# Kernel optimization log

Hardware: AMD Instinct MI355X
Metric: run time of the kernel (lower is better)

Reference implementation:

```python
import jax, jax.numpy as jnp
import numpy as np

BOS = 1          # BOS_TOK_IDX
PAD = 0          # PAD_TOK_IDX (embedding padding row zeroed)
NL = 2           # n_layers (both decoder and encoder)
H_DEC = 1024     # decoder hidden = enc.emb_size
H_ENC = 512      # encoder hidden per direction (out_size = 1024)


def lstm_cell(x, h, c, Wih, Whh, bih, bhh):
    # PyTorch gate order: i, f, g, o
    gates = x @ Wih.T + h @ Whh.T + bih + bhh
    i, f, g, o = jnp.split(gates, 4, axis=-1)
    c = jax.nn.sigmoid(f) * c + jax.nn.sigmoid(i) * jnp.tanh(g)
    h = jax.nn.sigmoid(o) * jnp.tanh(c)
    return h, c


def setup_inputs() -> dict:
    key = jax.random.key(0)
    ks = jax.random.split(key, 20)
    B, T_ENC, V, E = 32, 128, 32000, 512
    sd = 1.0 / np.sqrt(H_DEC)
    se = 1.0 / np.sqrt(H_ENC)
    u = lambda k, shape, s: jax.random.uniform(k, shape, jnp.float32, -s, s)
    emb_W = jax.random.normal(ks[0], (V, E), jnp.float32)
    emb_W = emb_W.at[PAD].set(0.0)  # padding_idx
    return {
        "enc_outs": jax.random.normal(ks[1], (B, T_ENC, 2 * H_ENC), jnp.float32),
        "enc_h": 0.1 * jax.random.normal(ks[2], (NL, B, H_DEC), jnp.float32),
        "enc_c": 0.1 * jax.random.normal(ks[3], (NL, B, H_DEC), jnp.float32),
        "max_len": 256,
        "emb_W": emb_W,
        # decoder LSTM (unidirectional, 2 layers; layer0 in=E, layer1 in=H_DEC)
        "dec_Wih0": u(ks[4], (4 * H_DEC, E), sd),
        "dec_Whh0": u(ks[5], (4 * H_DEC, H_DEC), sd),
        "dec_bih0": u(ks[6], (4 * H_DEC,), sd),
        "dec_bhh0": u(ks[7], (4 * H_DEC,), sd),
        "dec_Wih1": u(ks[8], (4 * H_DEC, H_DEC), sd),
        "dec_Whh1": u(ks[9], (4 * H_DEC, H_DEC), sd),
        "dec_bih1": u(ks[10], (4 * H_DEC,), sd),
        "dec_bhh1": u(ks[11], (4 * H_DEC,), sd),
        # encoder biLSTM, stacked [layer, dir]; input dim 1024 for both layers
        "enc_Wih": u(ks[12], (NL, 2, 4 * H_ENC, 2 * H_ENC), se),
        "enc_Whh": u(ks[13], (NL, 2, 4 * H_ENC, H_ENC), se),
        "enc_bih": u(ks[14], (NL, 2, 4 * H_ENC), se),
        "enc_bhh": u(ks[15], (NL, 2, 4 * H_ENC), se),
    }


def _run_dir(x, Wih, Whh, bih, bhh, reverse):
    # x: [B, T, D] -> ys: [B, T, H], final (h, c)
    B = x.shape[0]
    H = Whh.shape[-1]
    z = jnp.zeros((B, H), dtype=x.dtype)

    def step(carry, xt):
        h, c = lstm_cell(xt, carry[0], carry[1], Wih, Whh, bih, bhh)
        return (h, c), h

    (hT, cT), ys = jax.lax.scan(step, (z, z), jnp.swapaxes(x, 0, 1), reverse=reverse)
    return jnp.swapaxes(ys, 0, 1), hT, cT


def reference(enc_outs, enc_h, enc_c, max_len, emb_W,
              dec_Wih0, dec_Whh0, dec_bih0, dec_bhh0,
              dec_Wih1, dec_Whh1, dec_bih1, dec_bhh1,
              enc_Wih, enc_Whh, enc_bih, enc_bhh):
    B = enc_outs.shape[0]
    # dec_inps is never updated in the loop: always the BOS embedding (eval dropout = id)
    x0 = jnp.broadcast_to(emb_W[BOS], (B, emb_W.shape[1]))

    def dec_step(carry, _):
        h0, c0, h1, c1 = carry
        h0, c0 = lstm_cell(x0, h0, c0, dec_Wih0, dec_Whh0, dec_bih0, dec_bhh0)
        h1, c1 = lstm_cell(h0, h1, c1, dec_Wih1, dec_Whh1, dec_bih1, dec_bhh1)
        return (h0, c0, h1, c1), h1

    init = (enc_h[0], enc_c[0], enc_h[1], enc_c[1])
    _, result = jax.lax.scan(dec_step, init, None, length=max_len)  # [T, B, H_DEC]
    out = jnp.swapaxes(result, 0, 1)  # [B, T, H_DEC]

    # bidirectional encoder over the decoded sequence (pre_embedded, full lengths)
    for l in range(NL):
        yf, hf, cf = _run_dir(out, enc_Wih[l, 0], enc_Whh[l, 0], enc_bih[l, 0], enc_bhh[l, 0], False)
        yb, hb, cb = _run_dir(out, enc_Wih[l, 1], enc_Whh[l, 1], enc_bih[l, 1], enc_bhh[l, 1], True)
        out = jnp.concatenate([yf, yb], axis=-1)

    # to_dec_state: concat last-layer fwd/bwd states, expand over n_layers
    lnhn = jnp.concatenate([hf, hb], axis=1)  # [B, out_size]
    lncn = jnp.concatenate([cf, cb], axis=1)
    dec_h = jnp.broadcast_to(lnhn, (NL,) + lnhn.shape)
    dec_c = jnp.broadcast_to(lncn, (NL,) + lncn.shape)
    return out, dec_h, dec_c
```

## Files before the change

### kernel.cpp

```cpp
#include <hip/hip_runtime.h>


typedef _Float16 f16;
typedef _Float16 hvec8 __attribute__((ext_vector_type(8)));
typedef float fvec4 __attribute__((ext_vector_type(4)));

#define WS_H1   135168
#define WS_HE   266240
#define WS_DEC  397312
#define WS_Y0   17174528

__device__ __forceinline__ fvec4 mf(hvec8 a, hvec8 b, fvec4 c) {
    return __builtin_amdgcn_mfma_f32_16x16x32_f16(a, b, c, 0, 0, 0);
}

__device__ __forceinline__ hvec8 ldb8(const float* p) {
    hvec8 h;
#pragma unroll
    for (int j = 0; j < 8; ++j) h[j] = (f16)p[j];
    return h;
}

__device__ __forceinline__ hvec8 lda8(const f16* p) {
    hvec8 v;
    asm volatile("global_load_dwordx4 %0, %1, off sc1" : "=v"(v) : "v"(p));
    return v;
}
__device__ __forceinline__ void vm_wait() {
    asm volatile("s_waitcnt vmcnt(0)" ::: "memory");
    __builtin_amdgcn_sched_barrier(0);
}

__device__ __forceinline__ void st2(f16* p, float a, float b) {
    union { f16 h[2]; unsigned u; } x;
    x.h[0] = (f16)a; x.h[1] = (f16)b;
    __hip_atomic_store((unsigned*)p, x.u, __ATOMIC_RELAXED, __HIP_MEMORY_SCOPE_AGENT);
}

__device__ __forceinline__ float sigf(float x) { return 1.f / (1.f + __expf(-x)); }
__device__ __forceinline__ float thf(float x) {
    x = fminf(15.f, fmaxf(-15.f, x));
    float e = __expf(2.f * x);
    return (e - 1.f) / (e + 1.f);
}

#define RED(t, m, w, n)  red[(((t)*16 + (m))*132) + ((w)*16) + (n)]

__device__ __forceinline__ float sum8(const float* p) {
    return ((p[0] + p[16]) + (p[32] + p[48])) + ((p[64] + p[80]) + (p[96] + p[112]));
}

__global__ void __launch_bounds__(512, 1)
seq2seq_kernel(const float* __restrict__ enc_h, const float* __restrict__ enc_c,
               const float* __restrict__ emb_W,
               const float* __restrict__ dWih0, const float* __restrict__ dWhh0,
               const float* __restrict__ dbih0, const float* __restrict__ dbhh0,
               const float* __restrict__ dWih1, const float* __restrict__ dWhh1,
               const float* __restrict__ dbih1, const float* __restrict__ dbhh1,
               const float* __restrict__ eWih, const float* __restrict__ eWhh,
               const float* __restrict__ ebih, const float* __restrict__ ebhh,
               float* __restrict__ out, char* __restrict__ ws)
{
    const int tid  = threadIdx.x;
    const int wave = tid >> 6, lane = tid & 63;
    const int wg   = blockIdx.x;
    const int bg   = wg >> 7;
    const int layer= (wg >> 6) & 1;
    const int g2   = wg & 63;
    const int n16  = lane & 15;
    const int kq   = (lane >> 4) * 8;
    const int m    = n16;

    unsigned* flags  = (unsigned*)(out + 8388608);
    unsigned* myflag = flags + (size_t)wg * 64;

    f16* H1  = (f16*)(ws + WS_H1);
    f16* HE  = (f16*)(ws + WS_HE);
    f16* DEC = (f16*)(ws + WS_DEC);
    f16* Y0  = (f16*)(ws + WS_Y0);
    f16* H0R = Y0;

    __shared__ float red[64 * 132];
    __shared__ float cst[16][16];
    __shared__ float bias_l[64];

    unsigned cnt = 0;
    auto barpollW = [&](int base, int width, unsigned tgt) {
        if (lane == 0)
            __hip_atomic_store(myflag, tgt, __ATOMIC_RELAXED, __HIP_MEMORY_SCOPE_AGENT);
        const unsigned* p0 = flags + (size_t)(base + (lane & (width - 1))) * 64;
        for (;;) {
            unsigned a = __hip_atomic_load(p0, __ATOMIC_RELAXED, __HIP_MEMORY_SCOPE_AGENT);
            if (width > 64) {
                unsigned b = __hip_atomic_load(p0 + 64 * 64, __ATOMIC_RELAXED, __HIP_MEMORY_SCOPE_AGENT);
                a = a < b ? a : b;
                if (width > 128) {
                    unsigned c2 = __hip_atomic_load(p0 + 128 * 64, __ATOMIC_RELAXED, __HIP_MEMORY_SCOPE_AGENT);
                    unsigned d2 = __hip_atomic_load(p0 + 192 * 64, __ATOMIC_RELAXED, __HIP_MEMORY_SCOPE_AGENT);
                    a = a < c2 ? a : c2;
                    a = a < d2 ? a : d2;
                }
            }
            if (__all((int)(a >= tgt))) break;
            __builtin_amdgcn_s_sleep(1);
        }
    };
    auto barpoll2 = [&](int ownbase, int othbase, unsigned tgt, unsigned otgt) {
        if (lane == 0)
            __hip_atomic_store(myflag, tgt, __ATOMIC_RELAXED, __HIP_MEMORY_SCOPE_AGENT);
        const unsigned* p0 = flags + (size_t)(ownbase + lane) * 64;
        const unsigned* q0 = flags + (size_t)(othbase + lane) * 64;
        for (;;) {
            unsigned a = __hip_atomic_load(p0, __ATOMIC_RELAXED, __HIP_MEMORY_SCOPE_AGENT);
            unsigned b = __hip_atomic_load(q0, __ATOMIC_RELAXED, __HIP_MEMORY_SCOPE_AGENT);
            if (__all((int)((a >= tgt) && (b >= otgt)))) break;
            __builtin_amdgcn_s_sleep(1);
        }
    };

    const int u0 = g2 * 16;
    hvec8 bW[4][8];
    {
        const int gate = n16 >> 2, uu = n16 & 3;
        if (layer == 0) {
#pragma unroll
            for (int t = 0; t < 4; ++t) {
                const int r = gate * 1024 + u0 + t * 4 + uu;
#pragma unroll
                for (int s = 0; s < 4; ++s)
                    bW[t][s] = ldb8(dWhh0 + (size_t)r * 1024 + wave * 128 + s * 32 + kq);
            }
        } else {
#pragma unroll
            for (int t = 0; t < 4; ++t) {
                const int r = gate * 1024 + u0 + t * 4 + uu;
#pragma unroll
                for (int s = 0; s < 8; ++s) {
                    const int k1 = wave * 256 + s * 32;
                    bW[t][s] = (k1 < 1024)
                        ? ldb8(dWih1 + (size_t)r * 1024 + k1 + kq)
                        : ldb8(dWhh1 + (size_t)r * 1024 + (k1 - 1024) + kq);
                }
            }
        }
    }
    if (tid < 128) {
        const int j = tid >> 4, mm = tid & 15;
        const int b = bg * 16 + mm, u = u0 + 2 * j;
        const float* sc = enc_c + (size_t)(layer * 32 + b) * 1024 + u;
        const float* sh = enc_h + (size_t)(layer * 32 + b) * 1024 + u;
        cst[2 * j][mm]     = sc[0];
        cst[2 * j + 1][mm] = sc[1];
        if (layer == 0) st2(H0R + (size_t)(3 * 32 + b) * 1024 + u, sh[0], sh[1]);
        else            st2(H1  + (size_t)(32 + b) * 1024 + u, sh[0], sh[1]);
    }
    if (tid < 64) {
        const int t = tid >> 4, nn = tid & 15;
        const int r = (nn >> 2) * 1024 + u0 + t * 4 + (nn & 3);
        if (layer == 0) {
            const float* x0 = emb_W + 512;
            float s = dbih0[r] + dbhh0[r];
            const float* wr = dWih0 + (size_t)r * 512;
            for (int k = 0; k < 512; ++k) s += wr[k] * x0[k];
            bias_l[tid] = s;
        } else {
            bias_l[tid] = dbih1[r] + dbhh1[r];
        }
    }
    const int L0base = bg * 128, L1base = bg * 128 + 64;
    const int ownbase = layer ? L1base : L0base;
    const int othbase = layer ? L0base : L1base;
    __syncthreads();
    ++cnt;
    if (wave == 0) barpoll2(ownbase, othbase, cnt, cnt);
    __syncthreads();

    for (int n = 0; n <= 256; ++n) {
        const int prd = (n + 1) & 1;
        const int pwr = n & 1;
        const bool act = layer ? (n >= 1) : (n < 256);
        fvec4 acc[4];
#pragma unroll
        for (int i = 0; i < 4; ++i) acc[i] = 0;
        if (act) {
            hvec8 af[8];
            if (layer == 0) {
                const f16* a0 = H0R + (size_t)((((n - 1) & 3)) * 32 + bg * 16 + m) * 1024
                              + wave * 128 + kq;
#pragma unroll
                for (int s = 0; s < 4; ++s) af[s] = lda8(a0 + s * 32);
                vm_wait();
#pragma unroll
                for (int s = 0; s < 4; ++s)
#pragma unroll
                    for (int t = 0; t < 4; ++t) acc[t] = mf(af[s], bW[t][s], acc[t]);
            } else {
                const f16* b0 = H0R + (size_t)((((n - 1) & 3)) * 32 + bg * 16 + m) * 1024;
                const f16* b1 = H1 + (size_t)(pwr * 32 + bg * 16 + m) * 1024;
#pragma unroll
                for (int s = 0; s < 8; ++s) {
                    const int k1 = wave * 256 + s * 32;
                    af[s] = lda8(k1 < 1024 ? b0 + k1 + kq : b1 + (k1 - 1024) + kq);
                }
                vm_wait();
#pragma unroll
                for (int s = 0; s < 8; ++s)
#pragma unroll
                    for (int t = 0; t < 4; ++t) acc[t] = mf(af[s], bW[t][s], acc[t]);
            }
        }
        {
            const int mg = lane >> 4;
#pragma unroll
            for (int t = 0; t < 4; ++t)
#pragma unroll
                for (int r2 = 0; r2 < 4; ++r2)
                    RED(t, mg * 4 + r2, wave, n16) = acc[t][r2];
        }
        __syncthreads();
        float s0 = 0.f, s1 = 0.f;
        int   sm2 = 0, sj = 0;
        if (tid >= 64 && tid < 192 && act) {
            const int q = tid - 64;
            const int j = q >> 4, m2 = q & 15;
            float hh[2];
#pragma unroll
            for (int e = 0; e < 2; ++e) {
                const int uu = 2 * j + e, tt = uu >> 2, ul = uu & 3;
                const float* p = &RED(tt, m2, 0, ul);
                const float gi = sum8(p)      + bias_l[tt * 16 + ul];
                const float gf = sum8(p + 4)  + bias_l[tt * 16 + 4 + ul];
                const float gg = sum8(p + 8)  + bias_l[tt * 16 + 8 + ul];
                const float go = sum8(p + 12) + bias_l[tt * 16 + 12 + ul];
                float c = cst[uu][m2];
                c = sigf(gf) * c + sigf(gi) * thf(gg);
                hh[e] = sigf(go) * thf(c);
                cst[uu][m2] = c;
            }
            const int b = bg * 16 + m2, u = u0 + 2 * j;
            if (layer == 0) {
                st2(H0R + (size_t)((n & 3) * 32 + b) * 1024 + u, hh[0], hh[1]);
            } else {
                st2(H1 + (size_t)(prd * 32 + b) * 1024 + u, hh[0], hh[1]);
                s0 = hh[0]; s1 = hh[1]; sm2 = m2; sj = j;
            }
        }
        __syncthreads();
        ++cnt;
        if (wave == 0) {
            if (layer == 0) barpoll2(L0base, L1base, cnt, cnt < 2 ? 0u : cnt - 2);
            else            barpoll2(L1base, L0base, cnt, cnt);
        } else if (layer == 1 && tid >= 64 && tid < 192 && n >= 1) {
            st2(DEC + ((size_t)(n - 1) * 32 + bg * 16 + sm2) * 1024 + u0 + 2 * sj, s0, s1);
        }
        __syncthreads();
    }

    ++cnt;
    if (wave == 0) barpollW(0, 256, cnt);
    __syncthreads();
    if (wg >= 128) return;

    const int bg2 = wg >> 6;
    const int dir = (wg >> 5) & 1;
    const int ge  = wg & 31;
    const int ue0 = ge * 16;
    const int dbase = bg2 * 64 + dir * 32;
    float fdh0 = 0.f, fdh1 = 0.f, fdc0 = 0.f, fdc1 = 0.f;
    int   fdm2 = 0, fdj = 0;
    for (int l = 0; l < 2; ++l) {
        hvec8 bE[4][6];
        {
            const int gate = n16 >> 2, uu = n16 & 3;
            const float* Wih = eWih + (size_t)(l * 2 + dir) * 2048 * 1024;
            const float* Whh = eWhh + (size_t)(l * 2 + dir) * 2048 * 512;
#pragma unroll
            for (int t = 0; t < 4; ++t) {
                const int r = gate * 512 + ue0 + t * 4 + uu;
#pragma unroll
                for (int s = 0; s < 6; ++s) {
                    const int kb = wave * 192 + s * 32;
                    bE[t][s] = (kb < 1024)
                        ? ldb8(Wih + (size_t)r * 1024 + kb + kq)
                        : ldb8(Whh + (size_t)r * 512 + (kb - 1024) + kq);
                }
            }
        }
        if (tid < 64) {
            const int t = tid >> 4, nn = tid & 15;
            const int r = (nn >> 2) * 512 + ue0 + t * 4 + (nn & 3);
            bias_l[tid] = ebih[(size_t)(l * 2 + dir) * 2048 + r]
                        + ebhh[(size_t)(l * 2 + dir) * 2048 + r];
        }
        if (tid < 128) {
            const int j = tid >> 4, mm = tid & 15;
            cst[2 * j][mm] = 0.f;
            cst[2 * j + 1][mm] = 0.f;
            st2(HE + (size_t)((dir * 2 + 1) * 32 + bg2 * 16 + mm) * 512 + ue0 + 2 * j, 0.f, 0.f);
        }
        __syncthreads();
        ++cnt;
        if (wave == 0) barpollW(dbase, 32, cnt);
        __syncthreads();
        const f16* yprev = (l == 0) ? DEC : Y0;
        hvec8 ypf[6];
        {
            const int t0 = dir ? 255 : 0;
            const int b = bg2 * 16 + n16;
#pragma unroll
            for (int s = 0; s < 6; ++s) {
                const int kb = wave * 192 + s * 32;
                if (kb < 1024)
                    ypf[s] = lda8(yprev + ((size_t)t0 * 32 + b) * 1024 + kb + kq);
            }
        }
        for (int tau = 0; tau < 256; ++tau) {
            const int t = dir ? (255 - tau) : tau;
            const int prd = (tau + 1) & 1, pwr = tau & 1;
            const int b = bg2 * 16 + n16;
            hvec8 hef[6];
#pragma unroll
            for (int s = 0; s < 6; ++s) {
                const int kb = wave * 192 + s * 32;
                if (kb >= 1024)
                    hef[s] = lda8(HE + (size_t)((dir * 2 + prd) * 32 + b) * 512 + (kb - 1024) + kq);
            }
            vm_wait();
            fvec4 acc2[4];
#pragma unroll
            for (int i = 0; i < 4; ++i) acc2[i] = 0;
#pragma unroll
            for (int s = 0; s < 6; ++s) {
                const int kb = wave * 192 + s * 32;
                const hvec8 a = (kb < 1024) ? ypf[s] : hef[s];
                acc2[0] = mf(a, bE[0][s], acc2[0]);
                acc2[1] = mf(a, bE[1][s], acc2[1]);
                acc2[2] = mf(a, bE[2][s], acc2[2]);
                acc2[3] = mf(a, bE[3][s], acc2[3]);
            }
            if (tau < 255) {
                const int tn = dir ? (t - 1) : (t + 1);
#pragma unroll
                for (int s = 0; s < 6; ++s) {
                    const int kb = wave * 192 + s * 32;
                    if (kb < 1024)
                        ypf[s] = lda8(yprev + ((size_t)tn * 32 + b) * 1024 + kb + kq);
                }
            }
            const int mg = lane >> 4;
#pragma unroll
            for (int tt = 0; tt < 4; ++tt)
#pragma unroll
                for (int r2 = 0; r2 < 4; ++r2)
                    RED(tt, mg * 4 + r2, wave, n16) = acc2[tt][r2];
            __syncthreads();
            float dh0 = 0.f, dh1 = 0.f, dc0 = 0.f, dc1 = 0.f;
            int   dm2 = 0, dj = 0;
            if (tid >= 64 && tid < 192) {
                const int q = tid - 64;
                const int j = q >> 4, m2 = q & 15;
                float hh[2], cc[2];
#pragma unroll
                for (int e = 0; e < 2; ++e) {
                    const int uu = 2 * j + e, tt = uu >> 2, ul = uu & 3;
                    const float* p = &RED(tt, m2, 0, ul);
                    const float gi = sum8(p)      + bias_l[tt * 16 + ul];
                    const float gf = sum8(p + 4)  + bias_l[tt * 16 + 4 + ul];
                    const float gg = sum8(p + 8)  + bias_l[tt * 16 + 8 + ul];
                    const float go = sum8(p + 12) + bias_l[tt * 16 + 12 + ul];
                    float c = cst[uu][m2];
                    c = sigf(gf) * c + sigf(gi) * thf(gg);
                    hh[e] = sigf(go) * thf(c);
                    cc[e] = c;
                    cst[uu][m2] = c;
                }
                st2(HE + (size_t)((dir * 2 + pwr) * 32 + bg2 * 16 + m2) * 512 + ue0 + 2 * j,
                    hh[0], hh[1]);
                dh0 = hh[0]; dh1 = hh[1]; dc0 = cc[0]; dc1 = cc[1];
                dm2 = m2; dj = j;
            }
            __syncthreads();
            ++cnt;
            if (wave == 0) {
                if (!(l == 1 && tau == 255)) barpollW(dbase, 32, cnt);
            } else if (tid >= 64 && tid < 192) {
                const int b2 = bg2 * 16 + dm2, u = ue0 + 2 * dj;
                if (l == 0) {
                    st2(Y0 + ((size_t)t * 32 + b2) * 1024 + dir * 512 + u, dh0, dh1);
                } else {
                    float* o = out + ((size_t)b2 * 256 + t) * 1024 + dir * 512 + u;
                    o[0] = dh0; o[1] = dh1;
                    if (tau == 255) {
                        fdh0 = dh0; fdh1 = dh1;
                        fdc0 = dc0; fdc1 = dc1;
                        fdm2 = dm2; fdj = dj;
                    }
                }
            }
            __syncthreads();
        }
        if (l == 0) {
            __syncthreads();
            ++cnt;
            if (wave == 0) barpollW(bg2 * 64, 64, cnt);
            __syncthreads();
        }
    }
    __syncthreads();
    ++cnt;
    if (wave == 0) barpollW(0, 128, cnt);
    __syncthreads();
    if (tid >= 64 && tid < 192) {
        const int b2 = bg2 * 16 + fdm2;
        const int col = dir * 512 + ue0 + 2 * fdj;
        float* oh = out + 8388608 + (size_t)b2 * 1024 + col;
        float* oc = out + 8454144 + (size_t)b2 * 1024 + col;
        oh[0] = fdh0; oh[1] = fdh1;
        oh[32768] = fdh0; oh[32769] = fdh1;
        oc[0] = fdc0; oc[1] = fdc1;
        oc[32768] = fdc0; oc[32769] = fdc1;
    }
}

extern "C" void kernel_launch(void* const* d_in, const int* in_sizes, int n_in,
                              void* d_out, int out_size, void* d_ws, size_t ws_size,
                              hipStream_t stream) {
    (void)in_sizes; (void)n_in; (void)out_size; (void)ws_size;
    const float* enc_h = (const float*)d_in[1];
    const float* enc_c = (const float*)d_in[2];
    const float* emb_W = (const float*)d_in[4];
    const float* dWih0 = (const float*)d_in[5];
    const float* dWhh0 = (const float*)d_in[6];
    const float* dbih0 = (const float*)d_in[7];
    const float* dbhh0 = (const float*)d_in[8];
    const float* dWih1 = (const float*)d_in[9];
    const float* dWhh1 = (const float*)d_in[10];
    const float* dbih1 = (const float*)d_in[11];
    const float* dbhh1 = (const float*)d_in[12];
    const float* eWih  = (const float*)d_in[13];
    const float* eWhh  = (const float*)d_in[14];
    const float* ebih  = (const float*)d_in[15];
    const float* ebhh  = (const float*)d_in[16];
    float* outp = (float*)d_out;
    char* ws = (char*)d_ws;

    hipMemsetAsync((char*)d_out + 33554432, 0, 65536, stream);

    void* args[] = {&enc_h, &enc_c, &emb_W, &dWih0, &dWhh0, &dbih0, &dbhh0,
                    &dWih1, &dWhh1, &dbih1, &dbhh1, &eWih, &eWhh, &ebih, &ebhh,
                    &outp, &ws};
    hipLaunchCooperativeKernel((const void*)seq2seq_kernel, dim3(256), dim3(512),
                               args, 0, stream);
}
```

Before: 3.146 ms.

## Halve grid and interleave two batch halves with per-half flag barriers

Instead of assigning each 16-row batch group to separate workgroups (256 WGs), each of 128 WGs now processes both batch halves alternately, keeping two cell-state sets and two flag words per WG. Barriers become per-half point-to-point flags, so one half's compute can overlap another half's cross-WG synchronisation latency, and the DEC store moves into the compute path. This trades parallelism (half the CUs) for hiding barrier latency, and the encoder drops its Y prefetch in favour of loading the input each step.

```diff
diff --git a/kernel.cpp b/kernel.cpp
--- a/kernel.cpp
+++ b/kernel.cpp
@@ -64,8 +64,7 @@
     const int tid  = threadIdx.x;
     const int wave = tid >> 6, lane = tid & 63;
     const int wg   = blockIdx.x;
-    const int bg   = wg >> 7;
-    const int layer= (wg >> 6) & 1;
+    const int layer= wg >> 6;
     const int g2   = wg & 63;
     const int n16  = lane & 15;
     const int kq   = (lane >> 4) * 8;
@@ -81,41 +80,14 @@
     f16* H0R = Y0;
 
     __shared__ float red[64 * 132];
-    __shared__ float cst[16][16];
+    __shared__ float cst[2][16][16];
     __shared__ float bias_l[64];
 
-    unsigned cnt = 0;
-    auto barpollW = [&](int base, int width, unsigned tgt) {
-        if (lane == 0)
-            __hip_atomic_store(myflag, tgt, __ATOMIC_RELAXED, __HIP_MEMORY_SCOPE_AGENT);
-        const unsigned* p0 = flags + (size_t)(base + (lane & (width - 1))) * 64;
-        for (;;) {
-            unsigned a = __hip_atomic_load(p0, __ATOMIC_RELAXED, __HIP_MEMORY_SCOPE_AGENT);
-            if (width > 64) {
-                unsigned b = __hip_atomic_load(p0 + 64 * 64, __ATOMIC_RELAXED, __HIP_MEMORY_SCOPE_AGENT);
-                a = a < b ? a : b;
-                if (width > 128) {
-                    unsigned c2 = __hip_atomic_load(p0 + 128 * 64, __ATOMIC_RELAXED, __HIP_MEMORY_SCOPE_AGENT);
-                    unsigned d2 = __hip_atomic_load(p0 + 192 * 64, __ATOMIC_RELAXED, __HIP_MEMORY_SCOPE_AGENT);
-                    a = a < c2 ? a : c2;
-                    a = a < d2 ? a : d2;
-                }
-            }
-            if (__all((int)(a >= tgt))) break;
-            __builtin_amdgcn_s_sleep(1);
-        }
+    auto stflag = [&](int word, unsigned v) {
+        __hip_atomic_store(myflag + word * 16, v, __ATOMIC_RELAXED, __HIP_MEMORY_SCOPE_AGENT);
     };
-    auto barpoll2 = [&](int ownbase, int othbase, unsigned tgt, unsigned otgt) {
-        if (lane == 0)
-            __hip_atomic_store(myflag, tgt, __ATOMIC_RELAXED, __HIP_MEMORY_SCOPE_AGENT);
-        const unsigned* p0 = flags + (size_t)(ownbase + lane) * 64;
-        const unsigned* q0 = flags + (size_t)(othbase + lane) * 64;
-        for (;;) {
-            unsigned a = __hip_atomic_load(p0, __ATOMIC_RELAXED, __HIP_MEMORY_SCOPE_AGENT);
-            unsigned b = __hip_atomic_load(q0, __ATOMIC_RELAXED, __HIP_MEMORY_SCOPE_AGENT);
-            if (__all((int)((a >= tgt) && (b >= otgt)))) break;
-            __builtin_amdgcn_s_sleep(1);
-        }
+    auto ldflag = [&](const unsigned* p) {
+        return __hip_atomic_load(p, __ATOMIC_RELAXED, __HIP_MEMORY_SCOPE_AGENT);
     };
 
     const int u0 = g2 * 16;
@@ -146,13 +118,16 @@
     }
     if (tid < 128) {
         const int j = tid >> 4, mm = tid & 15;
-        const int b = bg * 16 + mm, u = u0 + 2 * j;
-        const float* sc = enc_c + (size_t)(layer * 32 + b) * 1024 + u;
-        const float* sh = enc_h + (size_t)(layer * 32 + b) * 1024 + u;
-        cst[2 * j][mm]     = sc[0];
-        cst[2 * j + 1][mm] = sc[1];
-        if (layer == 0) st2(H0R + (size_t)(3 * 32 + b) * 1024 + u, sh[0], sh[1]);
-        else            st2(H1  + (size_t)(32 + b) * 1024 + u, sh[0], sh[1]);
+#pragma unroll
+        for (int s = 0; s < 2; ++s) {
+            const int b = s * 16 + mm, u = u0 + 2 * j;
+            const float* sc = enc_c + (size_t)(layer * 32 + b) * 1024 + u;
+            const float* sh = enc_h + (size_t)(layer * 32 + b) * 1024 + u;
+            cst[s][2 * j][mm]     = sc[0];
+            cst[s][2 * j + 1][mm] = sc[1];
+            if (layer == 0) st2(H0R + (size_t)(3 * 32 + b) * 1024 + u, sh[0], sh[1]);
+            else            st2(H1  + (size_t)(32 + b) * 1024 + u, sh[0], sh[1]);
+        }
     }
     if (tid < 64) {
         const int t = tid >> 4, nn = tid & 15;
@@ -167,46 +142,52 @@
             bias_l[tid] = dbih1[r] + dbhh1[r];
         }
     }
-    const int L0base = bg * 128, L1base = bg * 128 + 64;
-    const int ownbase = layer ? L1base : L0base;
-    const int othbase = layer ? L0base : L1base;
+    const int ownbase = layer * 64, othbase = (layer ^ 1) * 64;
     __syncthreads();
-    ++cnt;
-    if (wave == 0) barpoll2(ownbase, othbase, cnt, cnt);
-    __syncthreads();
-
-    for (int n = 0; n <= 256; ++n) {
-        const int prd = (n + 1) & 1;
-        const int pwr = n & 1;
+    if (wave == 0) {
+        if (lane == 0) { stflag(0, 1u); stflag(1, 1u); }
+        const unsigned* p0 = flags + (size_t)(ownbase + lane) * 64;
+        for (;;) {
+            unsigned a = ldflag(p0), b = ldflag(p0 + 16);
+            if (__all((int)(a >= 1u && b >= 1u))) break;
+            __builtin_amdgcn_s_sleep(1);
+        }
+    }
+
+    for (int i = 0; i < 514; ++i) {
+        const int s = i & 1, n = i >> 1;
         const bool act = layer ? (n >= 1) : (n < 256);
+        __syncthreads();
+        if (wave == 0 && lane == 0 && i > 0)
+            stflag(s ^ 1, (unsigned)(((i - 1) >> 1) + 2));
         fvec4 acc[4];
 #pragma unroll
-        for (int i = 0; i < 4; ++i) acc[i] = 0;
+        for (int t = 0; t < 4; ++t) acc[t] = 0;
         if (act) {
             hvec8 af[8];
             if (layer == 0) {
-                const f16* a0 = H0R + (size_t)((((n - 1) & 3)) * 32 + bg * 16 + m) * 1024
+                const f16* a0 = H0R + (size_t)(((n - 1) & 3) * 32 + s * 16 + m) * 1024
                               + wave * 128 + kq;
 #pragma unroll
-                for (int s = 0; s < 4; ++s) af[s] = lda8(a0 + s * 32);
+                for (int sN = 0; sN < 4; ++sN) af[sN] = lda8(a0 + sN * 32);
                 vm_wait();
 #pragma unroll
-                for (int s = 0; s < 4; ++s)
-#pragma unroll
-                    for (int t = 0; t < 4; ++t) acc[t] = mf(af[s], bW[t][s], acc[t]);
+                for (int sN = 0; sN < 4; ++sN)
+#pragma unroll
+                    for (int t = 0; t < 4; ++t) acc[t] = mf(af[sN], bW[t][sN], acc[t]);
             } else {
-                const f16* b0 = H0R + (size_t)((((n - 1) & 3)) * 32 + bg * 16 + m) * 1024;
-                const f16* b1 = H1 + (size_t)(pwr * 32 + bg * 16 + m) * 1024;
-#pragma unroll
-                for (int s = 0; s < 8; ++s) {
-                    const int k1 = wave * 256 + s * 32;
-                    af[s] = lda8(k1 < 1024 ? b0 + k1 + kq : b1 + (k1 - 1024) + kq);
+                const f16* b0 = H0R + (size_t)(((n - 1) & 3) * 32 + s * 16 + m) * 1024;
+                const f16* b1 = H1 + (size_t)((n & 1) * 32 + s * 16 + m) * 1024;
+#pragma unroll
+                for (int sN = 0; sN < 8; ++sN) {
+                    const int k1 = wave * 256 + sN * 32;
+                    af[sN] = lda8(k1 < 1024 ? b0 + k1 + kq : b1 + (k1 - 1024) + kq);
                 }
                 vm_wait();
 #pragma unroll
-                for (int s = 0; s < 8; ++s)
-#pragma unroll
-                    for (int t = 0; t < 4; ++t) acc[t] = mf(af[s], bW[t][s], acc[t]);
+                for (int sN = 0; sN < 8; ++sN)
+#pragma unroll
+                    for (int t = 0; t < 4; ++t) acc[t] = mf(af[sN], bW[t][sN], acc[t]);
             }
         }
         {
@@ -218,9 +199,7 @@
                     RED(t, mg * 4 + r2, wave, n16) = acc[t][r2];
         }
         __syncthreads();
-        float s0 = 0.f, s1 = 0.f;
-        int   sm2 = 0, sj = 0;
-        if (tid >= 64 && tid < 192 && act) {
+        if (act && tid >= 64 && tid < 192) {
             const int q = tid - 64;
             const int j = q >> 4, m2 = q & 15;
             float hh[2];
@@ -232,42 +211,53 @@
                 const float gf = sum8(p + 4)  + bias_l[tt * 16 + 4 + ul];
                 const float gg = sum8(p + 8)  + bias_l[tt * 16 + 8 + ul];
                 const float go = sum8(p + 12) + bias_l[tt * 16 + 12 + ul];
-                float c = cst[uu][m2];
+                float c = cst[s][uu][m2];
                 c = sigf(gf) * c + sigf(gi) * thf(gg);
                 hh[e] = sigf(go) * thf(c);
-                cst[uu][m2] = c;
-            }
-            const int b = bg * 16 + m2, u = u0 + 2 * j;
+                cst[s][uu][m2] = c;
+            }
+            const int b = s * 16 + m2, u = u0 + 2 * j;
             if (layer == 0) {
                 st2(H0R + (size_t)((n & 3) * 32 + b) * 1024 + u, hh[0], hh[1]);
             } else {
-                st2(H1 + (size_t)(prd * 32 + b) * 1024 + u, hh[0], hh[1]);
-                s0 = hh[0]; s1 = hh[1]; sm2 = m2; sj = j;
-            }
-        }
-        __syncthreads();
-        ++cnt;
-        if (wave == 0) {
-            if (layer == 0) barpoll2(L0base, L1base, cnt, cnt < 2 ? 0u : cnt - 2);
-            else            barpoll2(L1base, L0base, cnt, cnt);
-        } else if (layer == 1 && tid >= 64 && tid < 192 && n >= 1) {
-            st2(DEC + ((size_t)(n - 1) * 32 + bg * 16 + sm2) * 1024 + u0 + 2 * sj, s0, s1);
-        }
-        __syncthreads();
-    }
-
-    ++cnt;
-    if (wave == 0) barpollW(0, 256, cnt);
+                st2(H1 + (size_t)(((n + 1) & 1) * 32 + b) * 1024 + u, hh[0], hh[1]);
+                st2(DEC + ((size_t)(n - 1) * 32 + b) * 1024 + u, hh[0], hh[1]);
+            }
+        }
+        if (wave == 0 && i + 1 < 514) {
+            const int s2 = (i + 1) & 1, n2 = (i + 1) >> 1;
+            const unsigned town = (unsigned)(n2 + 1);
+            const unsigned toth = layer ? (unsigned)(n2 + 1) : (unsigned)n2;
+            const unsigned* p0 = flags + (size_t)(ownbase + lane) * 64 + s2 * 16;
+            const unsigned* q0 = flags + (size_t)(othbase + lane) * 64 + s2 * 16;
+            for (;;) {
+                unsigned a = ldflag(p0), b = ldflag(q0);
+                if (__all((int)(a >= town && b >= toth))) break;
+                __builtin_amdgcn_s_sleep(1);
+            }
+        }
+    }
+
     __syncthreads();
-    if (wg >= 128) return;
-
-    const int bg2 = wg >> 6;
-    const int dir = (wg >> 5) & 1;
-    const int ge  = wg & 31;
+    if (wave == 0) {
+        if (lane == 0) { stflag(0, 259u); stflag(1, 259u); }
+        const unsigned* p0 = flags + (size_t)lane * 64;
+        const unsigned* p1 = p0 + (size_t)64 * 64;
+        for (;;) {
+            unsigned a = ldflag(p0), b = ldflag(p1);
+            if (__all((int)(a >= 259u && b >= 259u))) break;
+            __builtin_amdgcn_s_sleep(1);
+        }
+    }
+    __syncthreads();
+    if (wg >= 64) return;
+
+    const int dir = wg >> 5, ge = wg & 31;
     const int ue0 = ge * 16;
-    const int dbase = bg2 * 64 + dir * 32;
-    float fdh0 = 0.f, fdh1 = 0.f, fdc0 = 0.f, fdc1 = 0.f;
-    int   fdm2 = 0, fdj = 0;
+    const int dbase = dir * 32;
+    float f0h0 = 0.f, f0h1 = 0.f, f0c0 = 0.f, f0c1 = 0.f;
+    float f1h0 = 0.f, f1h1 = 0.f, f1c0 = 0.f, f1c1 = 0.f;
+    unsigned EB = 260;
     for (int l = 0; l < 2; ++l) {
         hvec8 bE[4][6];
         {
@@ -278,9 +268,9 @@
             for (int t = 0; t < 4; ++t) {
                 const int r = gate * 512 + ue0 + t * 4 + uu;
 #pragma unroll
-                for (int s = 0; s < 6; ++s) {
-                    const int kb = wave * 192 + s * 32;
-                    bE[t][s] = (kb < 1024)
+                for (int sN = 0; sN < 6; ++sN) {
+                    const int kb = wave * 192 + sN * 32;
+                    bE[t][sN] = (kb < 1024)
                         ? ldb8(Wih + (size_t)r * 1024 + kb + kq)
                         : ldb8(Whh + (size_t)r * 512 + (kb - 1024) + kq);
                 }
@@ -294,68 +284,60 @@
         }
         if (tid < 128) {
             const int j = tid >> 4, mm = tid & 15;
-            cst[2 * j][mm] = 0.f;
-            cst[2 * j + 1][mm] = 0.f;
-            st2(HE + (size_t)((dir * 2 + 1) * 32 + bg2 * 16 + mm) * 512 + ue0 + 2 * j, 0.f, 0.f);
+#pragma unroll
+            for (int s = 0; s < 2; ++s) {
+                cst[s][2 * j][mm] = 0.f;
+                cst[s][2 * j + 1][mm] = 0.f;
+                st2(HE + (size_t)((dir * 2 + 1) * 32 + s * 16 + mm) * 512 + ue0 + 2 * j,
+                    0.f, 0.f);
+            }
         }
         __syncthreads();
-        ++cnt;
-        if (wave == 0) barpollW(dbase, 32, cnt);
-        __syncthreads();
-        const f16* yprev = (l == 0) ? DEC : Y0;
-        hvec8 ypf[6];
-        {
-            const int t0 = dir ? 255 : 0;
-            const int b = bg2 * 16 + n16;
-#pragma unroll
-            for (int s = 0; s < 6; ++s) {
-                const int kb = wave * 192 + s * 32;
-                if (kb < 1024)
-                    ypf[s] = lda8(yprev + ((size_t)t0 * 32 + b) * 1024 + kb + kq);
-            }
-        }
-        for (int tau = 0; tau < 256; ++tau) {
+        if (wave == 0) {
+            if (lane == 0) { stflag(0, EB); stflag(1, EB); }
+            const unsigned* p0 = flags + (size_t)(dbase + (lane & 31)) * 64;
+            for (;;) {
+                unsigned a = ldflag(p0);
+                if (__all((int)(a >= EB))) break;
+                __builtin_amdgcn_s_sleep(1);
+            }
+        }
+        const f16* yprev = l ? Y0 : DEC;
+        for (int j2 = 0; j2 < 512; ++j2) {
+            const int s = j2 & 1, tau = j2 >> 1;
             const int t = dir ? (255 - tau) : tau;
             const int prd = (tau + 1) & 1, pwr = tau & 1;
-            const int b = bg2 * 16 + n16;
-            hvec8 hef[6];
-#pragma unroll
-            for (int s = 0; s < 6; ++s) {
-                const int kb = wave * 192 + s * 32;
-                if (kb >= 1024)
-                    hef[s] = lda8(HE + (size_t)((dir * 2 + prd) * 32 + b) * 512 + (kb - 1024) + kq);
+            __syncthreads();
+            if (wave == 0 && lane == 0 && j2 > 0)
+                stflag(s ^ 1, EB + (unsigned)(((j2 - 1) >> 1) + 1));
+            const int b = s * 16 + n16;
+            hvec8 af[6];
+#pragma unroll
+            for (int sN = 0; sN < 6; ++sN) {
+                const int kb = wave * 192 + sN * 32;
+                const f16* p = (kb < 1024)
+                    ? yprev + ((size_t)t * 32 + b) * 1024 + kb + kq
+                    : HE + (size_t)((dir * 2 + prd) * 32 + b) * 512 + (kb - 1024) + kq;
+                af[sN] = lda8(p);
             }
             vm_wait();
             fvec4 acc2[4];
 #pragma unroll
-            for (int i = 0; i < 4; ++i) acc2[i] = 0;
-#pragma unroll
-            for (int s = 0; s < 6; ++s) {
-                const int kb = wave * 192 + s * 32;
-                const hvec8 a = (kb < 1024) ? ypf[s] : hef[s];
-                acc2[0] = mf(a, bE[0][s], acc2[0]);
-                acc2[1] = mf(a, bE[1][s], acc2[1]);
-                acc2[2] = mf(a, bE[2][s], acc2[2]);
-                acc2[3] = mf(a, bE[3][s], acc2[3]);
-            }
-            if (tau < 255) {
-                const int tn = dir ? (t - 1) : (t + 1);
-#pragma unroll
-                for (int s = 0; s < 6; ++s) {
-                    const int kb = wave * 192 + s * 32;
-                    if (kb < 1024)
-                        ypf[s] = lda8(yprev + ((size_t)tn * 32 + b) * 1024 + kb + kq);
-                }
-            }
-            const int mg = lane >> 4;
-#pragma unroll
-            for (int tt = 0; tt < 4; ++tt)
-#pragma unroll
-                for (int r2 = 0; r2 < 4; ++r2)
-                    RED(tt, mg * 4 + r2, wave, n16) = acc2[tt][r2];
+            for (int t2 = 0; t2 < 4; ++t2) acc2[t2] = 0;
+#pragma unroll
+            for (int sN = 0; sN < 6; ++sN)
+#pragma unroll
+                for (int t2 = 0; t2 < 4; ++t2)
+                    acc2[t2] = mf(af[sN], bE[t2][sN], acc2[t2]);
+            {
+                const int mg = lane >> 4;
+#pragma unroll
+                for (int t2 = 0; t2 < 4; ++t2)
+#pragma unroll
+                    for (int r2 = 0; r2 < 4; ++r2)
+                        RED(t2, mg * 4 + r2, wave, n16) = acc2[t2][r2];
+            }
             __syncthreads();
-            float dh0 = 0.f, dh1 = 0.f, dc0 = 0.f, dc1 = 0.f;
-            int   dm2 = 0, dj = 0;
             if (tid >= 64 && tid < 192) {
                 const int q = tid - 64;
                 const int j = q >> 4, m2 = q & 15;
@@ -368,57 +350,77 @@
                     const float gf = sum8(p + 4)  + bias_l[tt * 16 + 4 + ul];
                     const float gg = sum8(p + 8)  + bias_l[tt * 16 + 8 + ul];
                     const float go = sum8(p + 12) + bias_l[tt * 16 + 12 + ul];
-                    float c = cst[uu][m2];
+                    float c = cst[s][uu][m2];
                     c = sigf(gf) * c + sigf(gi) * thf(gg);
                     hh[e] = sigf(go) * thf(c);
                     cc[e] = c;
-                    cst[uu][m2] = c;
-                }
-                st2(HE + (size_t)((dir * 2 + pwr) * 32 + bg2 * 16 + m2) * 512 + ue0 + 2 * j,
-                    hh[0], hh[1]);
-                dh0 = hh[0]; dh1 = hh[1]; dc0 = cc[0]; dc1 = cc[1];
-                dm2 = m2; dj = j;
-            }
-            __syncthreads();
-            ++cnt;
-            if (wave == 0) {
-                if (!(l == 1 && tau == 255)) barpollW(dbase, 32, cnt);
-            } else if (tid >= 64 && tid < 192) {
-                const int b2 = bg2 * 16 + dm2, u = ue0 + 2 * dj;
+                    cst[s][uu][m2] = c;
+                }
+                const int b2 = s * 16 + m2, u = ue0 + 2 * j;
+                st2(HE + (size_t)((dir * 2 + pwr) * 32 + b2) * 512 + u, hh[0], hh[1]);
                 if (l == 0) {
-                    st2(Y0 + ((size_t)t * 32 + b2) * 1024 + dir * 512 + u, dh0, dh1);
+                    st2(Y0 + ((size_t)t * 32 + b2) * 1024 + dir * 512 + u, hh[0], hh[1]);
                 } else {
                     float* o = out + ((size_t)b2 * 256 + t) * 1024 + dir * 512 + u;
-                    o[0] = dh0; o[1] = dh1;
+                    o[0] = hh[0]; o[1] = hh[1];
                     if (tau == 255) {
-                        fdh0 = dh0; fdh1 = dh1;
-                        fdc0 = dc0; fdc1 = dc1;
-                        fdm2 = dm2; fdj = dj;
+                        if (s == 0) { f0h0 = hh[0]; f0h1 = hh[1]; f0c0 = cc[0]; f0c1 = cc[1]; }
+                        else        { f1h0 = hh[0]; f1h1 = hh[1]; f1c0 = cc[0]; f1c1 = cc[1]; }
                     }
                 }
             }
+            if (wave == 0 && j2 + 1 < 512) {
+                const int s2 = (j2 + 1) & 1, tau2 = (j2 + 1) >> 1;
+                const unsigned tgt = EB + (unsigned)tau2;
+                const unsigned* p0 = flags + (size_t)(dbase + (lane & 31)) * 64 + s2 * 16;
+                for (;;) {
+                    unsigned a = ldflag(p0);
+                    if (__all((int)(a >= tgt))) break;
+                    __builtin_amdgcn_s_sleep(1);
+                }
+            }
+        }
+        __syncthreads();
+        if (l == 0) {
+            if (wave == 0) {
+                if (lane == 0) { stflag(0, EB + 257u); stflag(1, EB + 257u); }
+                const unsigned* p0 = flags + (size_t)lane * 64;
+                for (;;) {
+                    unsigned a = ldflag(p0);
+                    if (__all((int)(a >= EB + 257u))) break;
+                    __builtin_amdgcn_s_sleep(1);
+                }
+            }
             __syncthreads();
-        }
-        if (l == 0) {
-            __syncthreads();
-            ++cnt;
-            if (wave == 0) barpollW(bg2 * 64, 64, cnt);
-            __syncthreads();
-        }
-    }
-    __syncthreads();
-    ++cnt;
-    if (wave == 0) barpollW(0, 128, cnt);
+            EB += 258;
+        }
+    }
+    if (wave == 0) {
+        if (lane == 0) { stflag(0, EB + 257u); stflag(1, EB + 257u); }
+        const unsigned* p0 = flags + (size_t)lane * 64;
+        for (;;) {
+            unsigned a = ldflag(p0);
+            if (__all((int)(a >= EB + 257u))) break;
+            __builtin_amdgcn_s_sleep(1);
+        }
+    }
     __syncthreads();
     if (tid >= 64 && tid < 192) {
-        const int b2 = bg2 * 16 + fdm2;
-        const int col = dir * 512 + ue0 + 2 * fdj;
-        float* oh = out + 8388608 + (size_t)b2 * 1024 + col;
-        float* oc = out + 8454144 + (size_t)b2 * 1024 + col;
-        oh[0] = fdh0; oh[1] = fdh1;
-        oh[32768] = fdh0; oh[32769] = fdh1;
-        oc[0] = fdc0; oc[1] = fdc1;
-        oc[32768] = fdc0; oc[32769] = fdc1;
+        const int q = tid - 64;
+        const int j = q >> 4, m2 = q & 15;
+        const int col = dir * 512 + ue0 + 2 * j;
+        {
+            float* oh = out + 8388608 + (size_t)m2 * 1024 + col;
+            float* oc = out + 8454144 + (size_t)m2 * 1024 + col;
+            oh[0] = f0h0; oh[1] = f0h1; oh[32768] = f0h0; oh[32769] = f0h1;
+            oc[0] = f0c0; oc[1] = f0c1; oc[32768] = f0c0; oc[32769] = f0c1;
+        }
+        {
+            float* oh = out + 8388608 + (size_t)(16 + m2) * 1024 + col;
+            float* oc = out + 8454144 + (size_t)(16 + m2) * 1024 + col;
+            oh[0] = f1h0; oh[1] = f1h1; oh[32768] = f1h0; oh[32769] = f1h1;
+            oc[0] = f1c0; oc[1] = f1c1; oc[32768] = f1c0; oc[32769] = f1c1;
+        }
     }
 }
 
@@ -449,6 +451,6 @@
     void* args[] = {&enc_h, &enc_c, &emb_W, &dWih0, &dWhh0, &dbih0, &dbhh0,
                     &dWih1, &dWhh1, &dbih1, &dbhh1, &eWih, &eWhh, &ebih, &ebhh,
                     &outp, &ws};
-    hipLaunchCooperativeKernel((const void*)seq2seq_kernel, dim3(256), dim3(512),
+    hipLaunchCooperativeKernel((const void*)seq2seq_kernel, dim3(128), dim3(512),
                                args, 0, stream);
 }
```

New measurement: 5.041 ms. +60.2%, slower.
